# Optimization experiments

Measured on AMD Instinct MI355X. Metric: run time of the kernel, lower is better.

The kernel has to match this reference:

```python
import jax, jax.numpy as jnp
import numpy as np

# Involution-style aggregation (SAN Aggregation, pad_mode=0 / zero padding)
K, STRIDE, PAD, DIL = 3, 1, 1, 1


def setup_inputs() -> dict:
    key = jax.random.key(0)
    k1, k2 = jax.random.split(key)
    B, C, H, W = 8, 256, 64, 64
    WC = 16  # weight channels (channel groups share a kernel)
    OH = (H + 2 * PAD - (DIL * (K - 1) + 1)) // STRIDE + 1
    OW = (W + 2 * PAD - (DIL * (K - 1) + 1)) // STRIDE + 1
    x = jax.random.normal(k1, (B, C, H, W), dtype=jnp.float32)
    weight = jax.random.normal(k2, (B, WC, K * K, OH * OW), dtype=jnp.float32)
    return {"x": x, "weight": weight}


def reference(x, weight):
    B, C, H, W = x.shape
    _, WC, K2, _ = weight.shape
    OH = (H + 2 * PAD - (DIL * (K - 1) + 1)) // STRIDE + 1
    OW = (W + 2 * PAD - (DIL * (K - 1) + 1)) // STRIDE + 1
    G = C // WC  # channel groups sharing each dynamic kernel
    xp = jnp.pad(x, ((0, 0), (0, 0), (PAD, PAD), (PAD, PAD)))  # zero pad
    # weight per tap: [B, 1, WC, OH, OW] broadcast over groups
    w = weight.reshape(B, 1, WC, K2, OH, OW)
    out = jnp.zeros((B, G, WC, OH, OW), dtype=x.dtype)
    # fixed small K^2 loop over kernel taps; accumulate without materializing
    # the full unfolded [B, C, K^2, OH, OW] tensor
    for idx in range(K2):
        i, j = idx // K, idx % K
        xs = xp[:, :, i * DIL:i * DIL + (OH - 1) * STRIDE + 1:STRIDE,
                      j * DIL:j * DIL + (OW - 1) * STRIDE + 1:STRIDE]
        out = out + xs.reshape(B, G, WC, OH, OW) * w[:, :, :, idx]
    return out.reshape(B, C, OH, OW)
```

## Files before the change

kernel.cpp:

```cpp
#include <hip/hip_runtime.h>


#define NB 8
#define NC 256
#define NH 64
#define NW 64
#define NWC 16
#define NG 16
#define CPB 8
#define GSPLIT (NG / CPB)
#define LROW 68
#define LCH (18 * LROW)

__global__ __launch_bounds__(256, 4) void agg_kernel(const float* __restrict__ x,
                                                     const float* __restrict__ wt,
                                                     float* __restrict__ out) {
    __shared__ float lds[CPB * LCH];

    const int tid    = threadIdx.x;
    const int lane16 = tid & 15;
    const int row    = tid >> 4;
    const int bid    = blockIdx.x;
    const int strip  = bid & 3;
    const int wc     = (bid >> 2) & 15;
    const int gblk   = (bid >> 6) & (GSPLIT - 1);
    const int b      = bid >> 7;

    const int oh  = strip * 16 + row;
    const int ow0 = lane16 * 4;

    if (tid < CPB * 18) {
        *reinterpret_cast<float4*>(&lds[tid * LROW + NW]) = make_float4(0.f, 0.f, 0.f, 0.f);
    }

    const int r0 = strip * 16 - 1;
#pragma unroll
    for (int k = 0; k < 9; ++k) {
        const int f   = tid + k * 256;
        const int ch  = f / 288;
        const int rem = f - ch * 288;
        const int r   = rem >> 4;
        const int c4  = rem & 15;
        const int gr  = r0 + r;
        float4 v = make_float4(0.f, 0.f, 0.f, 0.f);
        if ((unsigned)gr < (unsigned)NH) {
            const int c = (gblk * CPB + ch) * NWC + wc;
            v = *reinterpret_cast<const float4*>(
                x + (((b * NC + c) * NH + gr) * NW) + c4 * 4);
        }
        *reinterpret_cast<float4*>(&lds[ch * LCH + r * LROW + c4 * 4]) = v;
    }

    float w[9][4];
    {
        const float* wp = wt + ((b * NWC + wc) * 9) * (NH * NW) + oh * NW + ow0;
#pragma unroll
        for (int idx = 0; idx < 9; ++idx) {
            float4 t = *reinterpret_cast<const float4*>(wp + idx * (NH * NW));
            w[idx][0] = t.x; w[idx][1] = t.y; w[idx][2] = t.z; w[idx][3] = t.w;
        }
    }

    __syncthreads();

    const bool has_left = (ow0 > 0);

#pragma unroll
    for (int ch = 0; ch < CPB; ++ch) {
        const int c = (gblk * CPB + ch) * NWC + wc;
        float acc[4] = {0.f, 0.f, 0.f, 0.f};

#pragma unroll
        for (int i = 0; i < 3; ++i) {
            const float* p = &lds[ch * LCH + (row + i) * LROW];
            float4 m = *reinterpret_cast<const float4*>(p + ow0);
            float l  = has_left ? p[ow0 - 1] : 0.f;
            float rt = p[ow0 + 4];
            float e[6];
            e[0] = l; e[1] = m.x; e[2] = m.y; e[3] = m.z; e[4] = m.w; e[5] = rt;
#pragma unroll
            for (int j = 0; j < 3; ++j) {
#pragma unroll
                for (int t = 0; t < 4; ++t) {
                    acc[t] += e[t + j] * w[i * 3 + j][t];
                }
            }
        }

        float4 o = make_float4(acc[0], acc[1], acc[2], acc[3]);
        *reinterpret_cast<float4*>(out + ((b * NC + c) * NH + oh) * NW + ow0) = o;
    }
}

extern "C" void kernel_launch(void* const* d_in, const int* in_sizes, int n_in,
                              void* d_out, int out_size, void* d_ws, size_t ws_size,
                              hipStream_t stream) {
    const float* x  = (const float*)d_in[0];
    const float* wt = (const float*)d_in[1];
    float* out      = (float*)d_out;

    dim3 grid(NB * NWC * GSPLIT * 4);
    dim3 block(256);
    agg_kernel<<<grid, block, 0, stream>>>(x, wt, out);
}
```

Before: 23.74 us.

## Retile aggregation so each block covers all channel groups for an 8-row strip

Each block now handles all 16 channel groups for one (batch, weight-channel, 8-row strip) tile instead of 8 groups over 16 rows. Each thread computes 8 output columns across 4 channels, reusing 72 weight registers, and the redundant per-block weight loads are removed. The LDS rows gain left and right zero padding, which drops the left-edge branch. Global loads are staged into registers before the LDS stores to overlap with the weight loads. The trade-offs are a larger halo fraction (10 rows loaded per 8 output rows), more registers, and fewer waves per SIMD (launch bound 3).

```diff
diff --git a/kernel.cpp b/kernel.cpp
--- a/kernel.cpp
+++ b/kernel.cpp
@@ -7,88 +7,102 @@
 #define NW 64
 #define NWC 16
 #define NG 16
-#define CPB 8
-#define GSPLIT (NG / CPB)
-#define LROW 68
-#define LCH (18 * LROW)
+#define LROW 72
+#define LCHR 10
+#define LCH (LCHR * LROW)
 
-__global__ __launch_bounds__(256, 4) void agg_kernel(const float* __restrict__ x,
+__global__ __launch_bounds__(256, 3) void agg_kernel(const float* __restrict__ x,
                                                      const float* __restrict__ wt,
                                                      float* __restrict__ out) {
-    __shared__ float lds[CPB * LCH];
+    __shared__ float lds[NG * LCH];
 
-    const int tid    = threadIdx.x;
-    const int lane16 = tid & 15;
-    const int row    = tid >> 4;
-    const int bid    = blockIdx.x;
-    const int strip  = bid & 3;
-    const int wc     = (bid >> 2) & 15;
-    const int gblk   = (bid >> 6) & (GSPLIT - 1);
-    const int b      = bid >> 7;
+    const int tid   = threadIdx.x;
+    const int l8    = tid & 7;
+    const int row   = (tid >> 3) & 7;
+    const int ch4   = tid >> 6;
+    const int bid   = blockIdx.x;
+    const int strip = bid & 7;
+    const int wc    = (bid >> 3) & 15;
+    const int b     = bid >> 7;
 
-    const int oh  = strip * 16 + row;
-    const int ow0 = lane16 * 4;
+    const int oh  = strip * 8 + row;
+    const int ow0 = l8 * 8;
 
-    if (tid < CPB * 18) {
-        *reinterpret_cast<float4*>(&lds[tid * LROW + NW]) = make_float4(0.f, 0.f, 0.f, 0.f);
-    }
-
-    const int r0 = strip * 16 - 1;
+    float4 sv[10];
+    int    laddr[10];
+    const int r0 = strip * 8 - 1;
 #pragma unroll
-    for (int k = 0; k < 9; ++k) {
+    for (int k = 0; k < 10; ++k) {
         const int f   = tid + k * 256;
-        const int ch  = f / 288;
-        const int rem = f - ch * 288;
+        const int ch  = f / 160;
+        const int rem = f - ch * 160;
         const int r   = rem >> 4;
         const int c4  = rem & 15;
         const int gr  = r0 + r;
         float4 v = make_float4(0.f, 0.f, 0.f, 0.f);
         if ((unsigned)gr < (unsigned)NH) {
-            const int c = (gblk * CPB + ch) * NWC + wc;
+            const int c = ch * NWC + wc;
             v = *reinterpret_cast<const float4*>(
                 x + (((b * NC + c) * NH + gr) * NW) + c4 * 4);
         }
-        *reinterpret_cast<float4*>(&lds[ch * LCH + r * LROW + c4 * 4]) = v;
+        sv[k]    = v;
+        laddr[k] = (ch * LCHR + r) * LROW + 4 + c4 * 4;
     }
 
-    float w[9][4];
+    float w[9][8];
     {
         const float* wp = wt + ((b * NWC + wc) * 9) * (NH * NW) + oh * NW + ow0;
 #pragma unroll
         for (int idx = 0; idx < 9; ++idx) {
-            float4 t = *reinterpret_cast<const float4*>(wp + idx * (NH * NW));
-            w[idx][0] = t.x; w[idx][1] = t.y; w[idx][2] = t.z; w[idx][3] = t.w;
+            float4 a = *reinterpret_cast<const float4*>(wp + idx * (NH * NW));
+            float4 q = *reinterpret_cast<const float4*>(wp + idx * (NH * NW) + 4);
+            w[idx][0] = a.x; w[idx][1] = a.y; w[idx][2] = a.z; w[idx][3] = a.w;
+            w[idx][4] = q.x; w[idx][5] = q.y; w[idx][6] = q.z; w[idx][7] = q.w;
         }
+    }
+
+#pragma unroll
+    for (int k = 0; k < 10; ++k) {
+        *reinterpret_cast<float4*>(&lds[laddr[k]]) = sv[k];
+    }
+    if (tid < NG * LCHR) {
+        const float4 z = make_float4(0.f, 0.f, 0.f, 0.f);
+        *reinterpret_cast<float4*>(&lds[tid * LROW])      = z;
+        *reinterpret_cast<float4*>(&lds[tid * LROW + 68]) = z;
     }
 
     __syncthreads();
 
-    const bool has_left = (ow0 > 0);
-
 #pragma unroll
-    for (int ch = 0; ch < CPB; ++ch) {
-        const int c = (gblk * CPB + ch) * NWC + wc;
-        float acc[4] = {0.f, 0.f, 0.f, 0.f};
+    for (int cc = 0; cc < 4; ++cc) {
+        const int g = ch4 * 4 + cc;
+        const float* pch = &lds[g * LCH];
+        float acc[8] = {0.f, 0.f, 0.f, 0.f, 0.f, 0.f, 0.f, 0.f};
 
 #pragma unroll
         for (int i = 0; i < 3; ++i) {
-            const float* p = &lds[ch * LCH + (row + i) * LROW];
-            float4 m = *reinterpret_cast<const float4*>(p + ow0);
-            float l  = has_left ? p[ow0 - 1] : 0.f;
-            float rt = p[ow0 + 4];
-            float e[6];
-            e[0] = l; e[1] = m.x; e[2] = m.y; e[3] = m.z; e[4] = m.w; e[5] = rt;
+            const float* p = pch + (row + i) * LROW;
+            float2 lo = *reinterpret_cast<const float2*>(p + ow0 + 2);
+            float4 m0 = *reinterpret_cast<const float4*>(p + ow0 + 4);
+            float4 m1 = *reinterpret_cast<const float4*>(p + ow0 + 8);
+            float2 hi = *reinterpret_cast<const float2*>(p + ow0 + 12);
+            float e[10];
+            e[0] = lo.y;
+            e[1] = m0.x; e[2] = m0.y; e[3] = m0.z; e[4] = m0.w;
+            e[5] = m1.x; e[6] = m1.y; e[7] = m1.z; e[8] = m1.w;
+            e[9] = hi.x;
 #pragma unroll
             for (int j = 0; j < 3; ++j) {
 #pragma unroll
-                for (int t = 0; t < 4; ++t) {
+                for (int t = 0; t < 8; ++t) {
                     acc[t] += e[t + j] * w[i * 3 + j][t];
                 }
             }
         }
 
-        float4 o = make_float4(acc[0], acc[1], acc[2], acc[3]);
-        *reinterpret_cast<float4*>(out + ((b * NC + c) * NH + oh) * NW + ow0) = o;
+        float* op = out + (((b * NC + g * NWC + wc) * NH + oh) * NW) + ow0;
+        *reinterpret_cast<float4*>(op)     = make_float4(acc[0], acc[1], acc[2], acc[3]);
+        *reinterpret_cast<float4*>(op + 4) = make_float4(acc[4], acc[5], acc[6], acc[7]);
     }
 }
 
@@ -99,7 +113,7 @@
     const float* wt = (const float*)d_in[1];
     float* out      = (float*)d_out;
 
-    dim3 grid(NB * NWC * GSPLIT * 4);
+    dim3 grid(NB * NWC * 8);
     dim3 block(256);
     agg_kernel<<<grid, block, 0, stream>>>(x, wt, out);
 }
```

Result: slower. 27.82 us (+17.2%).
